# Performance work log

Measured on AMD Instinct MI355X. Metric: run time of the kernel, lower is better.

Reference implementation:

```python
import jax, jax.numpy as jnp
import numpy as np

N, E, D, ED, H, OUT = 10000, 640000, 128, 64, 8, 128  # nodes, edges, node_dim, edge_dim, heads, out_features


def _lin_init(key, out_d, in_d):
    kw, kb = jax.random.split(key)
    lim = 1.0 / np.sqrt(in_d)
    W = jax.random.uniform(kw, (out_d, in_d), jnp.float32, -lim, lim)
    b = jax.random.uniform(kb, (out_d,), jnp.float32, -lim, lim)
    return W, b


def setup_inputs() -> dict:
    key = jax.random.key(0)
    ks = jax.random.split(key, 9)
    h = jax.random.normal(ks[0], (N, D), jnp.float32)
    t_ij = jax.random.normal(ks[1], (E, ED), jnp.float32)
    edge_index = jax.random.randint(ks[2], (2, E), 0, N, dtype=jnp.int64)
    Wq, bq = _lin_init(ks[3], D, D)
    Wk, bk = _lin_init(ks[4], D, D)
    W1, b1 = _lin_init(ks[5], OUT, D)   # MLP layer 1
    W2, b2 = _lin_init(ks[6], OUT, OUT)  # MLP layer 2
    Wre, bre = _lin_init(ks[7], D, ED)
    Wc, bc = _lin_init(ks[8], OUT, OUT)  # combine_heads
    return dict(h=h, t_ij=t_ij, edge_index=edge_index, Wq=Wq, bq=bq, Wk=Wk, bk=bk,
                W1=W1, b1=b1, W2=W2, b2=b2, Wre=Wre, bre=bre, Wc=Wc, bc=bc)


def reference(h, t_ij, edge_index, Wq, bq, Wk, bk, W1, b1, W2, b2, Wre, bre, Wc, bc):
    n_j, n_i = edge_index[0], edge_index[1]
    n_nodes = h.shape[0]
    # projections on nodes, then gather per edge
    q_i = (h @ Wq.T + bq).reshape(n_nodes, H, -1)[n_i]          # [E, H, d_h]
    k_j = (h @ Wk.T + bk).reshape(n_nodes, H, -1)[n_j]          # [E, H, d_h]
    v_nodes = jax.nn.silu(h @ W1.T + b1) @ W2.T + b2            # MLP(h): [N, OUT]
    v_j = v_nodes.reshape(n_nodes, H, -1)[n_j]                  # [E, H, d_h]
    re = jax.nn.silu(t_ij @ Wre.T + bre).reshape(t_ij.shape[0], H, -1)  # [E, H, d_h]
    # per-edge attention logits fused with edge features
    a_ij = (q_i * k_j * re).sum(-1, keepdims=True)              # [E, H, 1]
    # segment softmax grouped by destination node n_i
    m = jax.ops.segment_max(a_ij, n_i, num_segments=n_nodes)
    ex = jnp.exp(a_ij - m[n_i])
    s = jax.ops.segment_sum(ex, n_i, num_segments=n_nodes)
    a_i = ex / (s[n_i] + 1e-16)
    # note: original scales AFTER softmax
    a_i = a_i * (1.0 / np.sqrt(v_j.shape[2]))
    sea_ij = (a_i * v_j).reshape(a_i.shape[0], -1)              # [E, OUT]
    sea_ij = sea_ij @ Wc.T + bc                                 # combine_heads
    return sea_ij
```

## Files before the change

### kernel.cpp

```cpp
#include <hip/hip_runtime.h>

typedef __attribute__((ext_vector_type(8))) _Float16 half8;
typedef __attribute__((ext_vector_type(4))) float floatx4;

#define NN    10000
#define EE    640000
#define DD    128
#define EDD   64
#define HH    8
#define OUTD  128

__device__ __forceinline__ float fast_rcp(float x) { return __builtin_amdgcn_rcpf(x); }

__device__ __forceinline__ half8 cvt8h(const float* __restrict__ p) {
    const floatx4 a = *(const floatx4*)(const void*)p;
    const floatx4 b = *(const floatx4*)(const void*)(p + 4);
    half8 r;
    r[0] = (_Float16)a[0]; r[1] = (_Float16)a[1];
    r[2] = (_Float16)a[2]; r[3] = (_Float16)a[3];
    r[4] = (_Float16)b[0]; r[5] = (_Float16)b[1];
    r[6] = (_Float16)b[2]; r[7] = (_Float16)b[3];
    return r;
}

__device__ __forceinline__ int idx_is64(const int* __restrict__ eidx) {
    return ((eidx[1] | eidx[3] | eidx[5] | eidx[7]) == 0) ? 1 : 0;
}

__global__ void __launch_bounds__(256) k_prep(
    const float* __restrict__ Wq, const float* __restrict__ Wk,
    const float* __restrict__ W1, const float* __restrict__ W2,
    const float* __restrict__ Wc, const float* __restrict__ Wre,
    _Float16* __restrict__ w16, float* __restrict__ sf)
{
    const int gid = blockIdx.x * 256 + threadIdx.x;
    float v;
    if (gid < 16384)      v = Wq[gid];
    else if (gid < 32768) v = Wk[gid - 16384];
    else if (gid < 49152) v = W1[gid - 32768];
    else if (gid < 65536) v = W2[gid - 49152];
    else if (gid < 81920) v = Wc[gid - 65536];
    else                  v = Wre[gid - 81920];
    w16[gid] = (_Float16)v;
    if (gid < 80000) sf[gid] = 0.0f;
}

__global__ void __launch_bounds__(512) k_node(
    const float* __restrict__ h, const _Float16* __restrict__ w16,
    const float* __restrict__ bq, const float* __restrict__ bk,
    const float* __restrict__ b1, const float* __restrict__ b2,
    _Float16* __restrict__ qb, _Float16* __restrict__ kb,
    _Float16* __restrict__ vb)
{
    __shared__ _Float16 L[16 * 136];
    const int wave = threadIdx.x >> 6;
    const int lane = threadIdx.x & 63;
    const int c16 = lane & 15, q4 = lane >> 4;
    const int m0 = blockIdx.x * 16;

    const _Float16* Wq16 = w16;
    const _Float16* Wk16 = w16 + 16384;
    const _Float16* W116 = w16 + 32768;
    const _Float16* W216 = w16 + 49152;

    const float* hrow = h + (m0 + c16) * DD + q4 * 8;
    half8 af[4];
    af[0] = cvt8h(hrow);
    af[1] = cvt8h(hrow + 32);
    af[2] = cvt8h(hrow + 64);
    af[3] = cvt8h(hrow + 96);

#pragma unroll
    for (int i = 0; i < 3; ++i) {
        const int u = wave * 3 + i;
        const int pass = u >> 3;
        const int nt = u & 7;
        const _Float16* W = (pass == 0) ? Wq16 : ((pass == 1) ? Wk16 : W116);
        const float* B    = (pass == 0) ? bq   : ((pass == 1) ? bk   : b1);
        const int col = nt * 16 + c16;
        const float bias = B[col];
        floatx4 acc = {bias, bias, bias, bias};
        const _Float16* wr = W + col * DD + q4 * 8;
#pragma unroll
        for (int s = 0; s < 4; ++s)
            acc = __builtin_amdgcn_mfma_f32_16x16x32_f16(
                af[s], *(const half8*)(const void*)(wr + s * 32), acc, 0, 0, 0);
        if (pass < 2) {
            _Float16* dst = pass ? kb : qb;
#pragma unroll
            for (int r = 0; r < 4; ++r)
                dst[(m0 + q4 * 4 + r) * DD + col] = (_Float16)acc[r];
        } else {
#pragma unroll
            for (int r = 0; r < 4; ++r) {
                const float x = acc[r];
                L[(q4 * 4 + r) * 136 + col] = (_Float16)(x * fast_rcp(1.0f + __expf(-x)));
            }
        }
    }
    __syncthreads();

    half8 af2[4];
    const _Float16* l2 = L + c16 * 136 + q4 * 8;
#pragma unroll
    for (int s = 0; s < 4; ++s)
        af2[s] = *(const half8*)(const void*)(l2 + s * 32);
    {
        const int col = wave * 16 + c16;
        const float bias = b2[col];
        floatx4 acc = {bias, bias, bias, bias};
        const _Float16* wr = W216 + col * DD + q4 * 8;
#pragma unroll
        for (int s = 0; s < 4; ++s)
            acc = __builtin_amdgcn_mfma_f32_16x16x32_f16(
                af2[s], *(const half8*)(const void*)(wr + s * 32), acc, 0, 0, 0);
#pragma unroll
        for (int r = 0; r < 4; ++r)
            vb[(m0 + q4 * 4 + r) * DD + col] = (_Float16)acc[r];
    }
}

__global__ void __launch_bounds__(256) k_logits(
    const float* __restrict__ t, const int* __restrict__ eidx,
    const _Float16* __restrict__ Wre16, const float* __restrict__ bre,
    const _Float16* __restrict__ qb, const _Float16* __restrict__ kb,
    float* __restrict__ exf, float* __restrict__ sf)
{
    const int wave = threadIdx.x >> 6;
    const int lane = threadIdx.x & 63;
    const int c16 = lane & 15, q4 = lane >> 4;
    const int tile = blockIdx.x * 4 + wave;
    const int m0 = tile * 16;

    const int is64 = idx_is64(eidx);

    const float* trow = t + (m0 + c16) * EDD + q4 * 8;
    const half8 a0 = cvt8h(trow);
    const half8 a1 = cvt8h(trow + 32);

    int e_r[4], ni_r[4];
    const _Float16* qrow[4];
    const _Float16* krow[4];
#pragma unroll
    for (int r = 0; r < 4; ++r) {
        const int e = m0 + q4 * 4 + r;
        int nj, ni;
        if (is64) { nj = eidx[2 * e];      ni = eidx[2 * EE + 2 * e]; }
        else      { nj = eidx[e];          ni = eidx[EE + e]; }
        e_r[r] = e; ni_r[r] = ni;
        qrow[r] = qb + ni * DD + c16;
        krow[r] = kb + nj * DD + c16;
    }

    _Float16 qv[4], kv[4], qn[4], kn[4];
#pragma unroll
    for (int r = 0; r < 4; ++r) { qv[r] = qrow[r][0]; kv[r] = krow[r][0]; }

    for (int nt = 0; nt < 8; ++nt) {
        if (nt < 7) {
#pragma unroll
            for (int r = 0; r < 4; ++r) {
                qn[r] = qrow[r][(nt + 1) * 16];
                kn[r] = krow[r][(nt + 1) * 16];
            }
        }
        const int col = nt * 16 + c16;
        const float bias = bre[col];
        floatx4 acc = {bias, bias, bias, bias};
        const _Float16* wr = Wre16 + col * EDD + q4 * 8;
        acc = __builtin_amdgcn_mfma_f32_16x16x32_f16(
            a0, *(const half8*)(const void*)wr, acc, 0, 0, 0);
        acc = __builtin_amdgcn_mfma_f32_16x16x32_f16(
            a1, *(const half8*)(const void*)(wr + 32), acc, 0, 0, 0);

        float part[4];
#pragma unroll
        for (int r = 0; r < 4; ++r) {
            const float x = acc[r];
            const float re = x * fast_rcp(1.0f + __expf(-x));
            part[r] = re * (float)qv[r] * (float)kv[r];
        }
        for (int m = 1; m < 16; m <<= 1) {
            part[0] += __shfl_xor(part[0], m, 64);
            part[1] += __shfl_xor(part[1], m, 64);
            part[2] += __shfl_xor(part[2], m, 64);
            part[3] += __shfl_xor(part[3], m, 64);
        }
        if (c16 < 4) {
            const int r = c16;
            const float ex = __expf(part[r]);
            exf[e_r[r] * HH + nt] = ex;
            atomicAdd(&sf[ni_r[r] * HH + nt], ex);
        }
#pragma unroll
        for (int r = 0; r < 4; ++r) { qv[r] = qn[r]; kv[r] = kn[r]; }
    }
}

__global__ void __launch_bounds__(256, 8) k_out(
    const int* __restrict__ eidx, const float* __restrict__ exf,
    const float* __restrict__ sf, const _Float16* __restrict__ vb,
    const _Float16* __restrict__ Wc16, const float* __restrict__ bc,
    float* __restrict__ outp)
{
    __shared__ float Lf[4][16 * 68];
    const int wave = threadIdx.x >> 6;
    const int lane = threadIdx.x & 63;
    const int c16 = lane & 15, q4 = lane >> 4;
    const int tile = blockIdx.x * 4 + wave;
    const int m0 = tile * 16;

    const int is64 = idx_is64(eidx);

    const int e_a = m0 + c16;
    int nj, ni;
    if (is64) { nj = eidx[2 * e_a]; ni = eidx[2 * EE + 2 * e_a]; }
    else      { nj = eidx[e_a];     ni = eidx[EE + e_a]; }

    half8 af[4];
#pragma unroll
    for (int s = 0; s < 4; ++s) {
        const int h0 = s * 2 + (q4 >> 1);
        const float exv = exf[e_a * HH + h0];
        const float sv = sf[ni * HH + h0];
        const float asc = exv * fast_rcp(sv + 1e-16f) * 0.25f;
        const half8 v8 = *(const half8*)(const void*)(vb + nj * DD + s * 32 + q4 * 8);
        half8 y;
#pragma unroll
        for (int j = 0; j < 8; ++j)
            y[j] = (_Float16)((float)v8[j] * asc);
        af[s] = y;
    }

    floatx4 acc[8];
#pragma unroll
    for (int nt = 0; nt < 8; ++nt) {
        const int col = nt * 16 + c16;
        const float bias = bc[col];
        acc[nt] = (floatx4){bias, bias, bias, bias};
        const _Float16* wr = Wc16 + col * DD + q4 * 8;
#pragma unroll
        for (int s = 0; s < 4; ++s)
            acc[nt] = __builtin_amdgcn_mfma_f32_16x16x32_f16(
                af[s], *(const half8*)(const void*)(wr + s * 32), acc[nt], 0, 0, 0);
    }

    float* Lw = Lf[wave];
    float* ob = outp + (size_t)m0 * OUTD;
#pragma unroll
    for (int p = 0; p < 2; ++p) {
#pragma unroll
        for (int j = 0; j < 4; ++j)
#pragma unroll
            for (int r = 0; r < 4; ++r)
                Lw[(q4 * 4 + r) * 68 + j * 16 + c16] = acc[p * 4 + j][r];
#pragma unroll
        for (int tt = 0; tt < 4; ++tt) {
            const int idx = tt * 64 + lane;
            const int row = idx >> 4;
            const int c4 = (idx & 15) * 4;
            const floatx4 val = *(const floatx4*)(const void*)&Lw[row * 68 + c4];
            *(floatx4*)(void*)(ob + row * OUTD + p * 64 + c4) = val;
        }
    }
}

extern "C" void kernel_launch(void* const* d_in, const int* in_sizes, int n_in,
                              void* d_out, int out_size, void* d_ws, size_t ws_size,
                              hipStream_t stream) {
    (void)in_sizes; (void)n_in; (void)out_size; (void)ws_size;
    const float* h   = (const float*)d_in[0];
    const float* t   = (const float*)d_in[1];
    const int*   eidx= (const int*)d_in[2];
    const float* Wq  = (const float*)d_in[3];
    const float* bq  = (const float*)d_in[4];
    const float* Wk  = (const float*)d_in[5];
    const float* bk  = (const float*)d_in[6];
    const float* W1  = (const float*)d_in[7];
    const float* b1  = (const float*)d_in[8];
    const float* W2  = (const float*)d_in[9];
    const float* b2  = (const float*)d_in[10];
    const float* Wre = (const float*)d_in[11];
    const float* bre = (const float*)d_in[12];
    const float* Wc  = (const float*)d_in[13];
    const float* bc  = (const float*)d_in[14];
    float* out = (float*)d_out;

    char* ws = (char*)d_ws;
    _Float16* qb = (_Float16*)(ws);
    _Float16* kb = (_Float16*)(ws + 2560000);
    _Float16* vb = (_Float16*)(ws + 5120000);
    float*    exf= (float*)   (ws + 7680000);
    float*    sf = (float*)   (ws + 28160000);
    _Float16* w16= (_Float16*)(ws + 28480000);

    k_prep<<<dim3(352), dim3(256), 0, stream>>>(Wq, Wk, W1, W2, Wc, Wre, w16, sf);
    k_node<<<dim3(625), dim3(512), 0, stream>>>(h, w16, bq, bk, b1, b2, qb, kb, vb);
    k_logits<<<dim3(10000), dim3(256), 0, stream>>>(t, eidx, w16 + 81920, bre, qb, kb, exf, sf);
    k_out<<<dim3(10000), dim3(256), 0, stream>>>(eidx, exf, sf, vb, w16 + 65536, bc, out);
}
```

Before: 886.0 us.

## Transpose logits tile via LDS so each lane gathers contiguous q/k vectors

```diff
diff --git a/kernel.cpp b/kernel.cpp
--- a/kernel.cpp
+++ b/kernel.cpp
@@ -1,6 +1,7 @@
 #include <hip/hip_runtime.h>
 
 typedef __attribute__((ext_vector_type(8))) _Float16 half8;
+typedef __attribute__((ext_vector_type(4))) _Float16 h4v;
 typedef __attribute__((ext_vector_type(4))) float floatx4;
 
 #define NN    10000
@@ -126,6 +127,7 @@
     const _Float16* __restrict__ qb, const _Float16* __restrict__ kb,
     float* __restrict__ exf, float* __restrict__ sf)
 {
+    __shared__ float T[4][2][16 * 20];
     const int wave = threadIdx.x >> 6;
     const int lane = threadIdx.x & 63;
     const int c16 = lane & 15, q4 = lane >> 4;
@@ -134,36 +136,28 @@
 
     const int is64 = idx_is64(eidx);
 
+    const int e = m0 + c16;
+    int nj, ni;
+    if (is64) { nj = eidx[2 * e]; ni = eidx[2 * EE + 2 * e]; }
+    else      { nj = eidx[e];     ni = eidx[EE + e]; }
+
+    const _Float16* qrow = qb + ni * DD + q4 * 4;
+    const _Float16* krow = kb + nj * DD + q4 * 4;
+    h4v qv[8], kv[8];
+#pragma unroll
+    for (int nt = 0; nt < 8; ++nt) {
+        qv[nt] = *(const h4v*)(const void*)(qrow + nt * 16);
+        kv[nt] = *(const h4v*)(const void*)(krow + nt * 16);
+    }
+
     const float* trow = t + (m0 + c16) * EDD + q4 * 8;
     const half8 a0 = cvt8h(trow);
     const half8 a1 = cvt8h(trow + 32);
 
-    int e_r[4], ni_r[4];
-    const _Float16* qrow[4];
-    const _Float16* krow[4];
-#pragma unroll
-    for (int r = 0; r < 4; ++r) {
-        const int e = m0 + q4 * 4 + r;
-        int nj, ni;
-        if (is64) { nj = eidx[2 * e];      ni = eidx[2 * EE + 2 * e]; }
-        else      { nj = eidx[e];          ni = eidx[EE + e]; }
-        e_r[r] = e; ni_r[r] = ni;
-        qrow[r] = qb + ni * DD + c16;
-        krow[r] = kb + nj * DD + c16;
-    }
-
-    _Float16 qv[4], kv[4], qn[4], kn[4];
-#pragma unroll
-    for (int r = 0; r < 4; ++r) { qv[r] = qrow[r][0]; kv[r] = krow[r][0]; }
-
+    float exr[8];
+
+#pragma unroll
     for (int nt = 0; nt < 8; ++nt) {
-        if (nt < 7) {
-#pragma unroll
-            for (int r = 0; r < 4; ++r) {
-                qn[r] = qrow[r][(nt + 1) * 16];
-                kn[r] = krow[r][(nt + 1) * 16];
-            }
-        }
         const int col = nt * 16 + c16;
         const float bias = bre[col];
         floatx4 acc = {bias, bias, bias, bias};
@@ -173,27 +167,30 @@
         acc = __builtin_amdgcn_mfma_f32_16x16x32_f16(
             a1, *(const half8*)(const void*)(wr + 32), acc, 0, 0, 0);
 
-        float part[4];
+        float* Tw = T[wave][nt & 1];
 #pragma unroll
         for (int r = 0; r < 4; ++r) {
             const float x = acc[r];
-            const float re = x * fast_rcp(1.0f + __expf(-x));
-            part[r] = re * (float)qv[r] * (float)kv[r];
+            Tw[(q4 * 4 + r) * 20 + c16] = x * fast_rcp(1.0f + __expf(-x));
         }
-        for (int m = 1; m < 16; m <<= 1) {
-            part[0] += __shfl_xor(part[0], m, 64);
-            part[1] += __shfl_xor(part[1], m, 64);
-            part[2] += __shfl_xor(part[2], m, 64);
-            part[3] += __shfl_xor(part[3], m, 64);
-        }
-        if (c16 < 4) {
-            const int r = c16;
-            const float ex = __expf(part[r]);
-            exf[e_r[r] * HH + nt] = ex;
-            atomicAdd(&sf[ni_r[r] * HH + nt], ex);
-        }
-#pragma unroll
-        for (int r = 0; r < 4; ++r) { qv[r] = qn[r]; kv[r] = kn[r]; }
+        const floatx4 rev = *(const floatx4*)(const void*)&Tw[c16 * 20 + q4 * 4];
+
+        float part = rev[0] * (float)qv[nt][0] * (float)kv[nt][0]
+                   + rev[1] * (float)qv[nt][1] * (float)kv[nt][1]
+                   + rev[2] * (float)qv[nt][2] * (float)kv[nt][2]
+                   + rev[3] * (float)qv[nt][3] * (float)kv[nt][3];
+        part += __shfl_xor(part, 16, 64);
+        part += __shfl_xor(part, 32, 64);
+        const float ex = __expf(part);
+        exr[nt] = ex;
+        if (q4 == 0)
+            atomicAdd(&sf[ni * HH + nt], ex);
+    }
+
+    if (q4 == 0) {
+        float* eo = exf + (size_t)e * HH;
+        *(floatx4*)(void*)eo       = (floatx4){exr[0], exr[1], exr[2], exr[3]};
+        *(floatx4*)(void*)(eo + 4) = (floatx4){exr[4], exr[5], exr[6], exr[7]};
     }
 }
 
```

Result: no change. 899.8 us (+1.6%).
